# Performance work log

Hardware: AMD Instinct MI355X
Metric: run time of the kernel (lower is better)

## Reference

```python
import jax, jax.numpy as jnp
import numpy as np

N = 100000
E = 640000
IN_CH = 256
OUT_CH = 64
HID = 2 * OUT_CH  # 128


def setup_inputs() -> dict:
    key = jax.random.key(0)
    ks = jax.random.split(key, 8)
    x = jax.random.normal(ks[0], (N, IN_CH), dtype=jnp.float32)
    edge_index = jax.random.randint(ks[1], (2, E), 0, N, dtype=jnp.int32)
    s = 1.0 / np.sqrt(IN_CH)
    W1 = jax.random.uniform(ks[2], (IN_CH, HID), jnp.float32, -s, s)
    b1 = jnp.zeros((HID,), jnp.float32)
    s2 = 1.0 / np.sqrt(HID)
    W_mu = jax.random.uniform(ks[3], (HID, OUT_CH), jnp.float32, -s2, s2)
    b_mu = jnp.zeros((OUT_CH,), jnp.float32)
    W_ls = jax.random.uniform(ks[4], (HID, OUT_CH), jnp.float32, -s2, s2)
    b_ls = jnp.zeros((OUT_CH,), jnp.float32)
    return {"x": x, "W1": W1, "b1": b1, "W_mu": W_mu, "b_mu": b_mu,
            "W_ls": W_ls, "b_ls": b_ls, "edge_index": edge_index}


def _gcn_norm(edge_index, n_nodes):
    # PyG GCNConv default: add self-loops, symmetric normalization D^-1/2 A D^-1/2
    loops = jnp.arange(n_nodes, dtype=edge_index.dtype)
    src = jnp.concatenate([edge_index[0], loops])
    dst = jnp.concatenate([edge_index[1], loops])
    deg = jax.ops.segment_sum(jnp.ones_like(dst, jnp.float32), dst, num_segments=n_nodes)
    dinv = jnp.where(deg > 0, jax.lax.rsqrt(deg), 0.0)
    norm = dinv[src] * dinv[dst]  # [E+N]
    return src, dst, norm


def _gcn_conv(x, W, b, src, dst, norm, n_nodes):
    h = x @ W                                   # [N, F_out]
    msg = h[src] * norm[:, None]                # [E+N, F_out] gather
    out = jax.ops.segment_sum(msg, dst, num_segments=n_nodes)  # scatter-add
    return out + b


def reference(x, W1, b1, W_mu, b_mu, W_ls, b_ls, edge_index):
    src, dst, norm = _gcn_norm(edge_index, N)
    h = jax.nn.relu(_gcn_conv(x, W1, b1, src, dst, norm, N))
    mu = _gcn_conv(h, W_mu, b_mu, src, dst, norm, N)
    logstd = _gcn_conv(h, W_ls, b_ls, src, dst, norm, N)
    return mu, logstd
```

## Files before the change

kernel.cpp:

```cpp
#include <hip/hip_runtime.h>
#include <math.h>

#define NN 100000
#define EE 640000
#define INCH 256
#define HIDC 128
#define OUTC 64
#define NCHUNK ((NN + 255) / 256)

typedef __attribute__((ext_vector_type(8))) short short8;
typedef __attribute__((ext_vector_type(8))) unsigned short ushort8;
typedef __attribute__((ext_vector_type(4))) float floatx4;

__device__ __forceinline__ short f2bf(float f) {
    unsigned u = __float_as_uint(f);
    u += 0x7fff + ((u >> 16) & 1);
    return (short)(u >> 16);
}

__device__ __forceinline__ float bf2f(unsigned short u) {
    return __uint_as_float(((unsigned)u) << 16);
}

__device__ __forceinline__ unsigned pk2bf(float lo, float hi) {
    unsigned r;
    asm("v_cvt_pk_bf16_f32 %0, %1, %2" : "=v"(r) : "v"(lo), "v"(hi));
    return r;
}

__device__ __forceinline__ void async_copy16(const void* g, void* l) {
    __builtin_amdgcn_global_load_lds(
        (const __attribute__((address_space(1))) unsigned int*)g,
        (__attribute__((address_space(3))) unsigned int*)l,
        16, 0, 0);
}

__global__ void k_deg_zero(int* __restrict__ deg) {
    int i = blockIdx.x * 256 + threadIdx.x;
    if (i < NN) deg[i] = 0;
}

__global__ void k_deg_count(const int* __restrict__ dstp, int* __restrict__ deg) {
    int e = blockIdx.x * 256 + threadIdx.x;
    if (e < EE) atomicAdd(&deg[dstp[e]], 1);
}

__global__ __launch_bounds__(256) void k_scan1(const int* __restrict__ deg,
                                               int* __restrict__ partials) {
    int i = blockIdx.x * 256 + threadIdx.x;
    int v = (i < NN) ? deg[i] : 0;
    for (int o = 32; o; o >>= 1) v += __shfl_down(v, o, 64);
    __shared__ int sm[4];
    if ((threadIdx.x & 63) == 0) sm[threadIdx.x >> 6] = v;
    __syncthreads();
    if (threadIdx.x == 0) partials[blockIdx.x] = sm[0] + sm[1] + sm[2] + sm[3];
}

__global__ __launch_bounds__(512) void k_scan2(int* __restrict__ partials) {
    __shared__ int sm[512];
    int t = threadIdx.x;
    int v = (t < NCHUNK) ? partials[t] : 0;
    sm[t] = v;
    __syncthreads();
    for (int o = 1; o < 512; o <<= 1) {
        int add = (t >= o) ? sm[t - o] : 0;
        __syncthreads();
        sm[t] += add;
        __syncthreads();
    }
    if (t < NCHUNK) partials[t] = sm[t] - v;
}

__global__ __launch_bounds__(256) void k_scan3(const int* __restrict__ deg,
                                               const int* __restrict__ partials,
                                               int* __restrict__ row_off,
                                               int* __restrict__ cursor,
                                               float* __restrict__ dinv) {
    int t = threadIdx.x;
    int i = blockIdx.x * 256 + t;
    int v = (i < NN) ? deg[i] : 0;
    __shared__ int sm[256];
    sm[t] = v;
    __syncthreads();
    for (int o = 1; o < 256; o <<= 1) {
        int add = (t >= o) ? sm[t - o] : 0;
        __syncthreads();
        sm[t] += add;
        __syncthreads();
    }
    if (i < NN) {
        int excl = partials[blockIdx.x] + sm[t] - v;
        row_off[i] = excl;
        cursor[i] = excl;
        dinv[i] = rsqrtf((float)(v + 1));
    }
}

__global__ void k_fill(const int* __restrict__ srcp, const int* __restrict__ dstp,
                       int* __restrict__ cursor, int* __restrict__ esrc) {
    int e = blockIdx.x * 256 + threadIdx.x;
    if (e < EE) {
        int d = dstp[e];
        int pos = atomicAdd(&cursor[d], 1);
        esrc[pos] = srcp[e];
    }
}

__global__ void k_prep(const float* __restrict__ W1,
                       const float* __restrict__ Wmu, const float* __restrict__ bmu,
                       const float* __restrict__ Wls, const float* __restrict__ bls,
                       short* __restrict__ wt, short* __restrict__ wct,
                       float* __restrict__ bcat) {
    int i = blockIdx.x * 256 + threadIdx.x;
    if (i < 32768) {
        int n = i >> 8, k = i & 255;
        wt[i] = f2bf(W1[k * HIDC + n]);
    } else if (i < 32768 + 16384) {
        int j = i - 32768;
        int n = j >> 7, k = j & 127;
        float v = (n < OUTC) ? Wmu[k * OUTC + n] : Wls[k * OUTC + (n - OUTC)];
        wct[j] = f2bf(v);
    } else if (i < 32768 + 16384 + 128) {
        int c = i - (32768 + 16384);
        bcat[c] = (c < OUTC) ? bmu[c] : bls[c - OUTC];
    }
}

__global__ __launch_bounds__(256, 2) void k_mgemm1(const float* __restrict__ x,
                                                   const short* __restrict__ wt,
                                                   short* __restrict__ out) {
    __shared__ __align__(16) float xs[64 * 256];
    int wave = threadIdx.x >> 6;
    int lane = threadIdx.x & 63;
    int m = lane & 15, quad = lane >> 4;
    int rbase = blockIdx.x * 64;

#pragma unroll
    for (int i = 0; i < 16; i++) {
        int r = wave * 16 + i;
        int grow = rbase + r;
        if (grow >= NN) grow = NN - 1;
        const float* gsrc = x + (size_t)grow * INCH + ((lane ^ (r & 7)) << 2);
        float* ldst = xs + r * INCH;
        async_copy16(gsrc, ldst);
    }

    short8 bfr[2][8];
#pragma unroll
    for (int ct = 0; ct < 2; ct++)
#pragma unroll
        for (int k0 = 0; k0 < 8; k0++)
            bfr[ct][k0] = *(const short8*)(wt + (size_t)(wave * 32 + ct * 16 + m) * INCH
                                              + k0 * 32 + quad * 8);

    asm volatile("s_waitcnt vmcnt(0)" ::: "memory");
    __syncthreads();

    floatx4 acc[4][2];
#pragma unroll
    for (int rt = 0; rt < 4; rt++) { acc[rt][0] = (floatx4)(0.f); acc[rt][1] = (floatx4)(0.f); }

#pragma unroll
    for (int k0 = 0; k0 < 8; k0++) {
        int cbase = k0 * 8 + (quad << 1);
#pragma unroll
        for (int rt = 0; rt < 4; rt++) {
            int r = rt * 16 + m;
            int e = m & 7;
            const float* p0 = xs + r * INCH + (((cbase) ^ e) << 2);
            const float* p1 = xs + r * INCH + (((cbase + 1) ^ e) << 2);
            float4 f0 = *(const float4*)p0;
            float4 f1 = *(const float4*)p1;
            union { short8 s; unsigned u[4]; } a;
            a.u[0] = pk2bf(f0.x, f0.y); a.u[1] = pk2bf(f0.z, f0.w);
            a.u[2] = pk2bf(f1.x, f1.y); a.u[3] = pk2bf(f1.z, f1.w);
            acc[rt][0] = __builtin_amdgcn_mfma_f32_16x16x32_bf16(a.s, bfr[0][k0], acc[rt][0], 0, 0, 0);
            acc[rt][1] = __builtin_amdgcn_mfma_f32_16x16x32_bf16(a.s, bfr[1][k0], acc[rt][1], 0, 0, 0);
        }
    }

#pragma unroll
    for (int rt = 0; rt < 4; rt++) {
        int rs = rbase + rt * 16 + quad * 4;
#pragma unroll
        for (int ct = 0; ct < 2; ct++) {
            int c = wave * 32 + ct * 16 + m;
#pragma unroll
            for (int r = 0; r < 4; r++) {
                int rr = rs + r;
                if (rr < NN) out[(size_t)rr * HIDC + c] = f2bf(acc[rt][ct][r]);
            }
        }
    }
}

__global__ __launch_bounds__(256, 1) void k_mgemm2(const short* __restrict__ agg,
                                                   const short* __restrict__ wct,
                                                   const float* __restrict__ bcat,
                                                   float* __restrict__ out) {
    int wave = threadIdx.x >> 6;
    int lane = threadIdx.x & 63;
    int rhalf = wave & 1, chalf = wave >> 1;
    int m = lane & 15, quad = lane >> 4;
    int rbase = blockIdx.x * 64 + rhalf * 32;
    int r0c = min(rbase + m, NN - 1);
    int r1c = min(rbase + 16 + m, NN - 1);
    const short* ar0 = agg + (size_t)r0c * HIDC + quad * 8;
    const short* ar1 = agg + (size_t)r1c * HIDC + quad * 8;

    short8 pa0[4], pa1[4];
#pragma unroll
    for (int c = 0; c < 4; c++) {
        pa0[c] = *(const short8*)(ar0 + c * 32);
        pa1[c] = *(const short8*)(ar1 + c * 32);
    }
    __builtin_amdgcn_sched_barrier(0);

    const short* wbase = wct + quad * 8 + (size_t)m * HIDC + (size_t)(chalf * 4) * 16 * HIDC;
    floatx4 acc0[4], acc1[4];
#pragma unroll
    for (int i = 0; i < 4; i++) { acc0[i] = (floatx4)(0.f); acc1[i] = (floatx4)(0.f); }
#pragma unroll
    for (int k = 0; k < 4; k++) {
        const short* wq = wbase + k * 32;
#pragma unroll
        for (int nt = 0; nt < 4; nt++) {
            short8 b = *(const short8*)(wq + (size_t)nt * 16 * HIDC);
            acc0[nt] = __builtin_amdgcn_mfma_f32_16x16x32_bf16(pa0[k], b, acc0[nt], 0, 0, 0);
            acc1[nt] = __builtin_amdgcn_mfma_f32_16x16x32_bf16(pa1[k], b, acc1[nt], 0, 0, 0);
        }
    }
    int rs0 = rbase + quad * 4;
    int rs1 = rbase + 16 + quad * 4;
#pragma unroll
    for (int nt = 0; nt < 4; nt++) {
        int c = (chalf * 4 + nt) * 16 + m;
        float bv = bcat[c];
        float* obase = (c < OUTC) ? (out + c) : (out + (size_t)NN * OUTC + (c - OUTC));
#pragma unroll
        for (int r = 0; r < 4; r++) {
            int rr = rs0 + r;
            if (rr < NN) obase[(size_t)rr * OUTC] = acc0[nt][r] + bv;
            int rr2 = rs1 + r;
            if (rr2 < NN) obase[(size_t)rr2 * OUTC] = acc1[nt][r] + bv;
        }
    }
}

template <bool RELU>
__global__ __launch_bounds__(256) void k_gather(const short* __restrict__ feat,
                                                const int* __restrict__ esrc,
                                                const int* __restrict__ row_off,
                                                const int* __restrict__ deg,
                                                const float* __restrict__ dinv,
                                                const float* __restrict__ bias,
                                                short* __restrict__ out) {
    int gid = blockIdx.x * 256 + threadIdx.x;
    int d = gid >> 4;
    int l = threadIdx.x & 15;
    if (d >= NN) return;
    const ushort8* fp = (const ushort8*)feat;
    float dd = dinv[d];
    float sw = dd * dd;
    ushort8 sv = fp[(size_t)d * 16 + l];
    float acc[8];
#pragma unroll
    for (int i = 0; i < 8; i++) acc[i] = bf2f(sv[i]) * sw;
    int off = row_off[d];
    int cnt = deg[d];
    for (int base = 0; base < cnt; base += 16) {
        int mm = min(16, cnt - base);
        int sj = (l < mm) ? esrc[off + base + l] : 0;
        float dj = (l < mm) ? dinv[sj] : 0.f;
        int j = 0;
        for (; j + 4 <= mm; j += 4) {
            int s0 = __shfl(sj, j + 0, 16);
            int s1 = __shfl(sj, j + 1, 16);
            int s2 = __shfl(sj, j + 2, 16);
            int s3 = __shfl(sj, j + 3, 16);
            float n0 = __shfl(dj, j + 0, 16) * dd;
            float n1 = __shfl(dj, j + 1, 16) * dd;
            float n2 = __shfl(dj, j + 2, 16) * dd;
            float n3 = __shfl(dj, j + 3, 16) * dd;
            ushort8 v0 = fp[(size_t)s0 * 16 + l];
            ushort8 v1 = fp[(size_t)s1 * 16 + l];
            ushort8 v2 = fp[(size_t)s2 * 16 + l];
            ushort8 v3 = fp[(size_t)s3 * 16 + l];
#pragma unroll
            for (int i = 0; i < 8; i++) acc[i] = fmaf(bf2f(v0[i]), n0, acc[i]);
#pragma unroll
            for (int i = 0; i < 8; i++) acc[i] = fmaf(bf2f(v1[i]), n1, acc[i]);
#pragma unroll
            for (int i = 0; i < 8; i++) acc[i] = fmaf(bf2f(v2[i]), n2, acc[i]);
#pragma unroll
            for (int i = 0; i < 8; i++) acc[i] = fmaf(bf2f(v3[i]), n3, acc[i]);
        }
        if (j + 2 <= mm) {
            int s0 = __shfl(sj, j + 0, 16);
            int s1 = __shfl(sj, j + 1, 16);
            float n0 = __shfl(dj, j + 0, 16) * dd;
            float n1 = __shfl(dj, j + 1, 16) * dd;
            ushort8 v0 = fp[(size_t)s0 * 16 + l];
            ushort8 v1 = fp[(size_t)s1 * 16 + l];
#pragma unroll
            for (int i = 0; i < 8; i++) acc[i] = fmaf(bf2f(v0[i]), n0, acc[i]);
#pragma unroll
            for (int i = 0; i < 8; i++) acc[i] = fmaf(bf2f(v1[i]), n1, acc[i]);
            j += 2;
        }
        if (j < mm) {
            int s0 = __shfl(sj, j, 16);
            float n0 = __shfl(dj, j, 16) * dd;
            ushort8 v0 = fp[(size_t)s0 * 16 + l];
#pragma unroll
            for (int i = 0; i < 8; i++) acc[i] = fmaf(bf2f(v0[i]), n0, acc[i]);
        }
    }
    if (RELU) {
        float4 b0 = *(const float4*)(bias + l * 8);
        float4 b1 = *(const float4*)(bias + l * 8 + 4);
        acc[0] = fmaxf(acc[0] + b0.x, 0.f);
        acc[1] = fmaxf(acc[1] + b0.y, 0.f);
        acc[2] = fmaxf(acc[2] + b0.z, 0.f);
        acc[3] = fmaxf(acc[3] + b0.w, 0.f);
        acc[4] = fmaxf(acc[4] + b1.x, 0.f);
        acc[5] = fmaxf(acc[5] + b1.y, 0.f);
        acc[6] = fmaxf(acc[6] + b1.z, 0.f);
        acc[7] = fmaxf(acc[7] + b1.w, 0.f);
    }
    ushort8 o;
#pragma unroll
    for (int i = 0; i < 8; i++) o[i] = (unsigned short)f2bf(acc[i]);
    ((ushort8*)out)[(size_t)d * 16 + l] = o;
}

extern "C" void kernel_launch(void* const* d_in, const int* in_sizes, int n_in,
                              void* d_out, int out_size, void* d_ws, size_t ws_size,
                              hipStream_t stream) {
    const float* x   = (const float*)d_in[0];
    const float* W1  = (const float*)d_in[1];
    const float* b1  = (const float*)d_in[2];
    const float* Wmu = (const float*)d_in[3];
    const float* bmu = (const float*)d_in[4];
    const float* Wls = (const float*)d_in[5];
    const float* bls = (const float*)d_in[6];
    const int*   ei  = (const int*)d_in[7];
    const int* srcp = ei;
    const int* dstp = ei + EE;

    float* out = (float*)d_out;

    char* wsb = (char*)d_ws;
    short* bufA    = (short*)wsb;
    short* bufH    = bufA + (size_t)NN * HIDC;
    int*   deg     = (int*)(bufH + (size_t)NN * HIDC);
    int*   row_off = deg + NN;
    int*   cursor  = row_off + NN;
    float* dinv    = (float*)(cursor + NN);
    int*   esrc    = (int*)(dinv + NN);
    int*   partials = esrc + EE;
    short* wt      = (short*)(partials + NCHUNK + 1);
    short* wct     = wt + 128 * 256;
    float* bcat    = (float*)(wct + 128 * 128);

    const int nb_n = (NN + 255) / 256;
    const int nb_e = (EE + 255) / 256;
    const int nb_g = (NN * 16) / 256;
    const int nb_m = (NN + 63) / 64;

    k_deg_zero<<<nb_n, 256, 0, stream>>>(deg);
    k_deg_count<<<nb_e, 256, 0, stream>>>(dstp, deg);
    k_scan1<<<NCHUNK, 256, 0, stream>>>(deg, partials);
    k_scan2<<<1, 512, 0, stream>>>(partials);
    k_scan3<<<NCHUNK, 256, 0, stream>>>(deg, partials, row_off, cursor, dinv);
    k_fill<<<nb_e, 256, 0, stream>>>(srcp, dstp, cursor, esrc);
    k_prep<<<193, 256, 0, stream>>>(W1, Wmu, bmu, Wls, bls, wt, wct, bcat);

    k_mgemm1<<<nb_m, 256, 0, stream>>>(x, wt, bufA);
    k_gather<true><<<nb_g, 256, 0, stream>>>(bufA, esrc, row_off, deg, dinv, b1, bufH);

    k_gather<false><<<nb_g, 256, 0, stream>>>(bufH, esrc, row_off, deg, dinv, nullptr, bufA);
    k_mgemm2<<<nb_m, 256, 0, stream>>>(bufA, wct, bcat, out);
}
```

Measured before the change: 350.0 us.

## Fuse second-layer aggregation with mu/logstd GEMM via shared-memory tile

Replaces the separate second gather kernel and the output GEMM with one kernel. Each block aggregates 64 destination rows into an XOR-swizzled LDS tile, then runs MFMA against the concatenated mu/logstd weights and writes the outputs with bias. This removes the bf16 round trip of the aggregated hidden features through global memory and one launch. In exchange it has fewer blocks (64 rows per block, 16 lanes per row over 4 sequential rows) and a barrier between the gather and the GEMM, which may hurt latency hiding in the gather phase.

```diff
diff --git a/kernel.cpp b/kernel.cpp
--- a/kernel.cpp
+++ b/kernel.cpp
@@ -190,59 +190,6 @@
                 int rr = rs + r;
                 if (rr < NN) out[(size_t)rr * HIDC + c] = f2bf(acc[rt][ct][r]);
             }
-        }
-    }
-}
-
-__global__ __launch_bounds__(256, 1) void k_mgemm2(const short* __restrict__ agg,
-                                                   const short* __restrict__ wct,
-                                                   const float* __restrict__ bcat,
-                                                   float* __restrict__ out) {
-    int wave = threadIdx.x >> 6;
-    int lane = threadIdx.x & 63;
-    int rhalf = wave & 1, chalf = wave >> 1;
-    int m = lane & 15, quad = lane >> 4;
-    int rbase = blockIdx.x * 64 + rhalf * 32;
-    int r0c = min(rbase + m, NN - 1);
-    int r1c = min(rbase + 16 + m, NN - 1);
-    const short* ar0 = agg + (size_t)r0c * HIDC + quad * 8;
-    const short* ar1 = agg + (size_t)r1c * HIDC + quad * 8;
-
-    short8 pa0[4], pa1[4];
-#pragma unroll
-    for (int c = 0; c < 4; c++) {
-        pa0[c] = *(const short8*)(ar0 + c * 32);
-        pa1[c] = *(const short8*)(ar1 + c * 32);
-    }
-    __builtin_amdgcn_sched_barrier(0);
-
-    const short* wbase = wct + quad * 8 + (size_t)m * HIDC + (size_t)(chalf * 4) * 16 * HIDC;
-    floatx4 acc0[4], acc1[4];
-#pragma unroll
-    for (int i = 0; i < 4; i++) { acc0[i] = (floatx4)(0.f); acc1[i] = (floatx4)(0.f); }
-#pragma unroll
-    for (int k = 0; k < 4; k++) {
-        const short* wq = wbase + k * 32;
-#pragma unroll
-        for (int nt = 0; nt < 4; nt++) {
-            short8 b = *(const short8*)(wq + (size_t)nt * 16 * HIDC);
-            acc0[nt] = __builtin_amdgcn_mfma_f32_16x16x32_bf16(pa0[k], b, acc0[nt], 0, 0, 0);
-            acc1[nt] = __builtin_amdgcn_mfma_f32_16x16x32_bf16(pa1[k], b, acc1[nt], 0, 0, 0);
-        }
-    }
-    int rs0 = rbase + quad * 4;
-    int rs1 = rbase + 16 + quad * 4;
-#pragma unroll
-    for (int nt = 0; nt < 4; nt++) {
-        int c = (chalf * 4 + nt) * 16 + m;
-        float bv = bcat[c];
-        float* obase = (c < OUTC) ? (out + c) : (out + (size_t)NN * OUTC + (c - OUTC));
-#pragma unroll
-        for (int r = 0; r < 4; r++) {
-            int rr = rs0 + r;
-            if (rr < NN) obase[(size_t)rr * OUTC] = acc0[nt][r] + bv;
-            int rr2 = rs1 + r;
-            if (rr2 < NN) obase[(size_t)rr2 * OUTC] = acc1[nt][r] + bv;
         }
     }
 }
@@ -334,6 +281,132 @@
     ((ushort8*)out)[(size_t)d * 16 + l] = o;
 }
 
+__global__ __launch_bounds__(256, 4) void k_gagg2(const short* __restrict__ feat,
+                                                  const int* __restrict__ esrc,
+                                                  const int* __restrict__ row_off,
+                                                  const int* __restrict__ deg,
+                                                  const float* __restrict__ dinv,
+                                                  const short* __restrict__ wct,
+                                                  const float* __restrict__ bcat,
+                                                  float* __restrict__ out) {
+    __shared__ __align__(16) short as_[64 * 128];
+    int tid = threadIdx.x;
+    int g = tid >> 4;
+    int l = tid & 15;
+    int rbase = blockIdx.x * 64;
+    const ushort8* fp = (const ushort8*)feat;
+
+#pragma unroll
+    for (int i = 0; i < 4; i++) {
+        int lr = g * 4 + i;
+        int d = rbase + lr;
+        float acc[8];
+#pragma unroll
+        for (int q = 0; q < 8; q++) acc[q] = 0.f;
+        if (d < NN) {
+            float dd = dinv[d];
+            float sw = dd * dd;
+            ushort8 sv = fp[(size_t)d * 16 + l];
+#pragma unroll
+            for (int q = 0; q < 8; q++) acc[q] = bf2f(sv[q]) * sw;
+            int off = row_off[d];
+            int cnt = deg[d];
+            for (int base = 0; base < cnt; base += 16) {
+                int mm = min(16, cnt - base);
+                int sj = (l < mm) ? esrc[off + base + l] : 0;
+                float dj = (l < mm) ? dinv[sj] : 0.f;
+                int j = 0;
+                for (; j + 4 <= mm; j += 4) {
+                    int s0 = __shfl(sj, j + 0, 16);
+                    int s1 = __shfl(sj, j + 1, 16);
+                    int s2 = __shfl(sj, j + 2, 16);
+                    int s3 = __shfl(sj, j + 3, 16);
+                    float n0 = __shfl(dj, j + 0, 16) * dd;
+                    float n1 = __shfl(dj, j + 1, 16) * dd;
+                    float n2 = __shfl(dj, j + 2, 16) * dd;
+                    float n3 = __shfl(dj, j + 3, 16) * dd;
+                    ushort8 v0 = fp[(size_t)s0 * 16 + l];
+                    ushort8 v1 = fp[(size_t)s1 * 16 + l];
+                    ushort8 v2 = fp[(size_t)s2 * 16 + l];
+                    ushort8 v3 = fp[(size_t)s3 * 16 + l];
+#pragma unroll
+                    for (int q = 0; q < 8; q++) acc[q] = fmaf(bf2f(v0[q]), n0, acc[q]);
+#pragma unroll
+                    for (int q = 0; q < 8; q++) acc[q] = fmaf(bf2f(v1[q]), n1, acc[q]);
+#pragma unroll
+                    for (int q = 0; q < 8; q++) acc[q] = fmaf(bf2f(v2[q]), n2, acc[q]);
+#pragma unroll
+                    for (int q = 0; q < 8; q++) acc[q] = fmaf(bf2f(v3[q]), n3, acc[q]);
+                }
+                if (j + 2 <= mm) {
+                    int s0 = __shfl(sj, j + 0, 16);
+                    int s1 = __shfl(sj, j + 1, 16);
+                    float n0 = __shfl(dj, j + 0, 16) * dd;
+                    float n1 = __shfl(dj, j + 1, 16) * dd;
+                    ushort8 v0 = fp[(size_t)s0 * 16 + l];
+                    ushort8 v1 = fp[(size_t)s1 * 16 + l];
+#pragma unroll
+                    for (int q = 0; q < 8; q++) acc[q] = fmaf(bf2f(v0[q]), n0, acc[q]);
+#pragma unroll
+                    for (int q = 0; q < 8; q++) acc[q] = fmaf(bf2f(v1[q]), n1, acc[q]);
+                    j += 2;
+                }
+                if (j < mm) {
+                    int s0 = __shfl(sj, j, 16);
+                    float n0 = __shfl(dj, j, 16) * dd;
+                    ushort8 v0 = fp[(size_t)s0 * 16 + l];
+#pragma unroll
+                    for (int q = 0; q < 8; q++) acc[q] = fmaf(bf2f(v0[q]), n0, acc[q]);
+                }
+            }
+        }
+        ushort8 o;
+#pragma unroll
+        for (int q = 0; q < 8; q++) o[q] = (unsigned short)f2bf(acc[q]);
+        *(ushort8*)(as_ + (size_t)lr * 128 + ((l ^ (lr & 7)) << 3)) = o;
+    }
+    __syncthreads();
+
+    int wave = tid >> 6;
+    int lane = tid & 63;
+    int rhalf = wave & 1, chalf = wave >> 1;
+    int m = lane & 15, quad = lane >> 4;
+    int lr0 = rhalf * 32 + m;
+    int lr1 = rhalf * 32 + 16 + m;
+
+    const short* wbase = wct + quad * 8 + (size_t)m * HIDC + (size_t)(chalf * 4) * 16 * HIDC;
+    floatx4 acc0[4], acc1[4];
+#pragma unroll
+    for (int i = 0; i < 4; i++) { acc0[i] = (floatx4)(0.f); acc1[i] = (floatx4)(0.f); }
+#pragma unroll
+    for (int k = 0; k < 4; k++) {
+        short8 a0 = *(const short8*)(as_ + (size_t)lr0 * 128 + (((k * 4 + quad) ^ (lr0 & 7)) << 3));
+        short8 a1 = *(const short8*)(as_ + (size_t)lr1 * 128 + (((k * 4 + quad) ^ (lr1 & 7)) << 3));
+        const short* wq = wbase + k * 32;
+#pragma unroll
+        for (int nt = 0; nt < 4; nt++) {
+            short8 b = *(const short8*)(wq + (size_t)nt * 16 * HIDC);
+            acc0[nt] = __builtin_amdgcn_mfma_f32_16x16x32_bf16(a0, b, acc0[nt], 0, 0, 0);
+            acc1[nt] = __builtin_amdgcn_mfma_f32_16x16x32_bf16(a1, b, acc1[nt], 0, 0, 0);
+        }
+    }
+    int rs0 = rbase + rhalf * 32 + quad * 4;
+    int rs1 = rbase + rhalf * 32 + 16 + quad * 4;
+#pragma unroll
+    for (int nt = 0; nt < 4; nt++) {
+        int c = (chalf * 4 + nt) * 16 + m;
+        float bv = bcat[c];
+        float* obase = (c < OUTC) ? (out + c) : (out + (size_t)NN * OUTC + (c - OUTC));
+#pragma unroll
+        for (int r = 0; r < 4; r++) {
+            int rr = rs0 + r;
+            if (rr < NN) obase[(size_t)rr * OUTC] = acc0[nt][r] + bv;
+            int rr2 = rs1 + r;
+            if (rr2 < NN) obase[(size_t)rr2 * OUTC] = acc1[nt][r] + bv;
+        }
+    }
+}
+
 extern "C" void kernel_launch(void* const* d_in, const int* in_sizes, int n_in,
                               void* d_out, int out_size, void* d_ws, size_t ws_size,
                               hipStream_t stream) {
@@ -379,6 +452,5 @@
     k_mgemm1<<<nb_m, 256, 0, stream>>>(x, wt, bufA);
     k_gather<true><<<nb_g, 256, 0, stream>>>(bufA, esrc, row_off, deg, dinv, b1, bufH);
 
-    k_gather<false><<<nb_g, 256, 0, stream>>>(bufH, esrc, row_off, deg, dinv, nullptr, bufA);
-    k_mgemm2<<<nb_m, 256, 0, stream>>>(bufA, wct, bcat, out);
-}
+    k_gagg2<<<nb_m, 256, 0, stream>>>(bufH, esrc, row_off, deg, dinv, wct, bcat, out);
+}
```

After: 351.8 us. About the same (+0.5%).
